# Kernel tuning notes

Measured on AMD Instinct MI355X. Metric: run time of the kernel, lower is better.

The kernel has to match this reference:

```python
import jax, jax.numpy as jnp
import numpy as np

B, T, E, H = 4, 2048, 1024, 16
HD = E // H  # 64


def setup_inputs() -> dict:
    key = jax.random.key(0)
    ks = jax.random.split(key, 7)
    s = 0.02
    return {
        "values": jax.random.normal(ks[0], (B, T, E), jnp.float32),
        "keys": jax.random.normal(ks[1], (B, T, E), jnp.float32),
        "query": jax.random.normal(ks[2], (B, T, E), jnp.float32),
        "Wv": jax.random.normal(ks[3], (HD, HD), jnp.float32) * s,
        "Wk": jax.random.normal(ks[4], (HD, HD), jnp.float32) * s,
        "Wq": jax.random.normal(ks[5], (HD, HD), jnp.float32) * s,
        "Wo": jax.random.normal(ks[6], (E, E), jnp.float32) * s,
    }


def _proj_split(x, W):
    # x: [B,T,E] -> per-head projection with shared [HD,HD] weight -> [B,H,T,HD]
    xh = x.reshape(B, T, H, HD)
    return jnp.einsum("bthd,ed->bhte", xh, W)  # torch Linear: x @ W.T


def reference(values, keys, query, Wv, Wk, Wq, Wo):
    v = _proj_split(values, Wv)   # [B,H,T,HD]
    k = _proj_split(keys, Wk)
    q = _proj_split(query, Wq)
    scale = 1.0 / np.sqrt(HD).astype(np.float32)
    scores = jnp.einsum("bhqd,bhkd->bhqk", q, k) * scale  # [B,H,T,T]
    probs = jax.nn.softmax(scores, axis=-1)
    attn = jnp.einsum("bhqk,bhkd->bhqd", probs, v)        # [B,H,T,HD]
    out = attn.transpose(0, 2, 1, 3).reshape(B, T, E)      # combine heads
    return out @ Wo.T
```

## Files before the change

kernel.cpp:

```cpp
#include <hip/hip_runtime.h>


typedef __bf16 bf16x8 __attribute__((ext_vector_type(8)));
typedef float f32x4 __attribute__((ext_vector_type(4)));
typedef float f32x16 __attribute__((ext_vector_type(16)));
typedef unsigned int u32x2v __attribute__((ext_vector_type(2)));
typedef unsigned int u32x4v __attribute__((ext_vector_type(4)));

#define DEVI static __device__ __forceinline__

constexpr int Bc = 4, Tc = 2048, Ec = 1024, HDc = 64;
constexpr int BHc = 64;

DEVI unsigned short f2bf(float f) {
  unsigned int u = __builtin_bit_cast(unsigned int, f);
  u += 0x7fffu + ((u >> 16) & 1u);
  return (unsigned short)(u >> 16);
}

DEVI int swzf(int row) { return (row & 7) ^ ((row >> 3) & 3); }

DEVI bf16x8 lds_frag(const unsigned short* base, int row, int chunk) {
  const char* p = reinterpret_cast<const char*>(base) + row * 128 + ((chunk ^ swzf(row)) * 16);
  return *reinterpret_cast<const bf16x8*>(p);
}
DEVI void lds_store16(unsigned short* base, int row, int ci, uint4 v) {
  char* p = reinterpret_cast<char*>(base) + row * 128 + ((ci ^ swzf(row)) * 16);
  *reinterpret_cast<uint4*>(p) = v;
}
DEVI uint4 pack8(float4 a, float4 b) {
  uint4 o;
  o.x = f2bf(a.x) | ((unsigned)f2bf(a.y) << 16);
  o.y = f2bf(a.z) | ((unsigned)f2bf(a.w) << 16);
  o.z = f2bf(b.x) | ((unsigned)f2bf(b.y) << 16);
  o.w = f2bf(b.z) | ((unsigned)f2bf(b.w) << 16);
  return o;
}

DEVI unsigned cvt_pk_bf16(float lo, float hi) {
  unsigned r;
  asm("v_cvt_pk_bf16_f32 %0, %1, %2" : "=v"(r) : "v"(lo), "v"(hi));
  return r;
}
DEVI float exp2_fast(float x) {
  float r;
  asm("v_exp_f32 %0, %1" : "=v"(r) : "v"(x));
  return r;
}
DEVI void plswap(unsigned& a, unsigned& b) {
#if __has_builtin(__builtin_amdgcn_permlane32_swap)
  u32x2v r = __builtin_amdgcn_permlane32_swap(a, b, false, false);
  a = r.x; b = r.y;
#else
  int lane = threadIdx.x & 63;
  unsigned sa = (unsigned)__shfl_xor((int)a, 32), sb = (unsigned)__shfl_xor((int)b, 32);
  unsigned na = (lane < 32) ? a : sb;
  unsigned nb = (lane < 32) ? sa : b;
  a = na; b = nb;
#endif
}
DEVI float halfsum(float x) {
  unsigned a = __builtin_bit_cast(unsigned, x), b = a;
  plswap(a, b);
  return __builtin_bit_cast(float, a) + __builtin_bit_cast(float, b);
}

DEVI void gload16(const unsigned short* g, unsigned short* l) {
  __builtin_amdgcn_global_load_lds(
      (const __attribute__((address_space(1))) void*)g,
      (__attribute__((address_space(3))) void*)l, 16, 0, 0);
}

__global__ __launch_bounds__(256) void proj3_kernel(
    const float* __restrict__ xv, const float* __restrict__ xk,
    const float* __restrict__ xq, const float* __restrict__ Wv,
    const float* __restrict__ Wk, const float* __restrict__ Wq,
    const float* __restrict__ Wo, unsigned short* __restrict__ ov,
    unsigned short* __restrict__ ok, unsigned short* __restrict__ oq,
    unsigned short* __restrict__ wob, float qscale) {
  if (blockIdx.z == 3) {
    int cb = blockIdx.y * (int)gridDim.x + blockIdx.x;
    if (cb < 1024) {
      size_t i = (size_t)cb * 1024 + (size_t)threadIdx.x * 4;
      float4 f = *reinterpret_cast<const float4*>(Wo + i);
      uint2 o;
      o.x = f2bf(f.x) | ((unsigned)f2bf(f.y) << 16);
      o.y = f2bf(f.z) | ((unsigned)f2bf(f.w) << 16);
      *reinterpret_cast<uint2*>(wob + i) = o;
    }
    return;
  }
  const int which = blockIdx.z;
  const float* x = which == 0 ? xv : which == 1 ? xk : xq;
  const float* W = which == 0 ? Wv : which == 1 ? Wk : Wq;
  unsigned short* out = which == 0 ? ov : which == 1 ? ok : oq;
  const int transposed = (which == 0);
  const float wscale = (which == 2) ? qscale : 1.0f;

  __shared__ __align__(16) unsigned short Xl[64 * 64];
  __shared__ __align__(16) unsigned short Wl[64 * 64];
  const int tid = threadIdx.x;
  const int bh = blockIdx.y, t0 = blockIdx.x * 64;
  const int b = bh >> 4, h = bh & 15;
  const float* xbase = x + (size_t)(b * Tc + t0) * Ec + h * HDc;

#pragma unroll
  for (int it = 0; it < 2; ++it) {
    int ch = tid + it * 256;
    int row = ch >> 3, ci = ch & 7;
    float4 wa = *reinterpret_cast<const float4*>(W + row * 64 + ci * 8);
    float4 wb = *reinterpret_cast<const float4*>(W + row * 64 + ci * 8 + 4);
    wa.x *= wscale; wa.y *= wscale; wa.z *= wscale; wa.w *= wscale;
    wb.x *= wscale; wb.y *= wscale; wb.z *= wscale; wb.w *= wscale;
    lds_store16(Wl, row, ci, pack8(wa, wb));
    float4 xa = *reinterpret_cast<const float4*>(xbase + (size_t)row * Ec + ci * 8);
    float4 xb = *reinterpret_cast<const float4*>(xbase + (size_t)row * Ec + ci * 8 + 4);
    lds_store16(Xl, row, ci, pack8(xa, xb));
  }
  __syncthreads();

  const int lane = tid & 63, wv = tid >> 6;
  const int c16 = lane & 15, hi = lane >> 4;
  f32x4 acc[4];
#pragma unroll
  for (int nb = 0; nb < 4; ++nb) acc[nb] = {0.f, 0.f, 0.f, 0.f};
  if (!transposed) {
#pragma unroll
    for (int c = 0; c < 2; ++c) {
      bf16x8 aX = lds_frag(Xl, 16 * wv + c16, 4 * c + hi);
#pragma unroll
      for (int nb = 0; nb < 4; ++nb) {
        bf16x8 bW = lds_frag(Wl, 16 * nb + c16, 4 * c + hi);
        acc[nb] = __builtin_amdgcn_mfma_f32_16x16x32_bf16(aX, bW, acc[nb], 0, 0, 0);
      }
    }
#pragma unroll
    for (int nb = 0; nb < 4; ++nb)
#pragma unroll
      for (int r = 0; r < 4; ++r) {
        int t = t0 + 16 * wv + 4 * hi + r;
        int e = 16 * nb + c16;
        out[(size_t)(bh * Tc + t) * HDc + e] = f2bf(acc[nb][r]);
      }
  } else {
#pragma unroll
    for (int c = 0; c < 2; ++c) {
      bf16x8 aW = lds_frag(Wl, 16 * wv + c16, 4 * c + hi);
#pragma unroll
      for (int nb = 0; nb < 4; ++nb) {
        bf16x8 bX = lds_frag(Xl, 16 * nb + c16, 4 * c + hi);
        acc[nb] = __builtin_amdgcn_mfma_f32_16x16x32_bf16(aW, bX, acc[nb], 0, 0, 0);
      }
    }
#pragma unroll
    for (int nb = 0; nb < 4; ++nb)
#pragma unroll
      for (int r = 0; r < 4; ++r) {
        int e = 16 * wv + 4 * hi + r;
        int t = t0 + 16 * nb + c16;
        out[(size_t)(bh * HDc + e) * Tc + t] = f2bf(acc[nb][r]);
      }
  }
}

DEVI void stage_kv(const unsigned short* __restrict__ Kp,
                   const unsigned short* __restrict__ Vp, int kt,
                   unsigned short* Kl, unsigned short* Vl, int wv, int lane) {
#pragma unroll
  for (int j = 0; j < 2; ++j) {
    const int base = (4 * j + wv) * 64;
    const int slot = base + lane;
    const int row = slot >> 3;
    const int sc = ((slot & 7) ^ swzf(row)) * 8;
    gload16(Kp + (size_t)(kt * 64 + row) * 64 + sc, Kl + base * 8);
    gload16(Vp + (size_t)row * Tc + kt * 64 + sc, Vl + base * 8);
  }
}

DEVI float exp_sum_pf(f32x16& s0, f32x16& s1, bf16x8 pf[4]) {
#pragma unroll
  for (int i = 0; i < 16; ++i) s0[i] = exp2_fast(s0[i]);
#pragma unroll
  for (int i = 0; i < 16; ++i) s1[i] = exp2_fast(s1[i]);
  float t[16];
#pragma unroll
  for (int i = 0; i < 16; ++i) t[i] = s0[i] + s1[i];
#pragma unroll
  for (int i = 0; i < 8; ++i) t[i] += t[i + 8];
#pragma unroll
  for (int i = 0; i < 4; ++i) t[i] += t[i + 4];
  float rs = (t[0] + t[1]) + (t[2] + t[3]);
  unsigned w0[8], w1[8];
#pragma unroll
  for (int i = 0; i < 8; ++i) w0[i] = cvt_pk_bf16(s0[2 * i], s0[2 * i + 1]);
#pragma unroll
  for (int i = 0; i < 8; ++i) w1[i] = cvt_pk_bf16(s1[2 * i], s1[2 * i + 1]);
  plswap(w0[0], w0[2]); plswap(w0[1], w0[3]); plswap(w0[4], w0[6]); plswap(w0[5], w0[7]);
  plswap(w1[0], w1[2]); plswap(w1[1], w1[3]); plswap(w1[4], w1[6]); plswap(w1[5], w1[7]);
  pf[0] = __builtin_bit_cast(bf16x8, (u32x4v){w0[0], w0[1], w0[2], w0[3]});
  pf[1] = __builtin_bit_cast(bf16x8, (u32x4v){w0[4], w0[5], w0[6], w0[7]});
  pf[2] = __builtin_bit_cast(bf16x8, (u32x4v){w1[0], w1[1], w1[2], w1[3]});
  pf[3] = __builtin_bit_cast(bf16x8, (u32x4v){w1[4], w1[5], w1[6], w1[7]});
  return rs;
}

__global__ __launch_bounds__(256, 2) void attn_kernel(
    const unsigned short* __restrict__ Qb_, const unsigned short* __restrict__ Kb_,
    const unsigned short* __restrict__ Vtb_, unsigned short* __restrict__ O) {
  __shared__ __align__(16) unsigned short KV[4][2][64 * 64];
  const int tid = threadIdx.x, lane = tid & 63, wv = tid >> 6;
  const int c32 = lane & 31, hi = lane >> 5;
  const int flat = blockIdx.y * (int)gridDim.x + blockIdx.x;
  const int logical = (flat & 7) * 64 + (flat >> 3);
  const int q0 = (logical & 7) * 256, bh = logical >> 3;
  const int b = bh >> 4, h = bh & 15;
  const unsigned short* Qp = Qb_ + (size_t)bh * Tc * HDc;
  const unsigned short* Kp = Kb_ + (size_t)bh * Tc * HDc;
  const unsigned short* Vp = Vtb_ + (size_t)bh * HDc * Tc;

  const int tA = q0 + 64 * wv + c32, tB = tA + 32;
  bf16x8 qfA[4], qfB[4];
#pragma unroll
  for (int c = 0; c < 4; ++c) {
    qfA[c] = *reinterpret_cast<const bf16x8*>(Qp + (size_t)tA * HDc + 16 * c + 8 * hi);
    qfB[c] = *reinterpret_cast<const bf16x8*>(Qp + (size_t)tB * HDc + 16 * c + 8 * hi);
  }

  stage_kv(Kp, Vp, 0, KV[0][0], KV[0][1], wv, lane);
  stage_kv(Kp, Vp, 1, KV[1][0], KV[1][1], wv, lane);

  f32x16 aA0, aA1, aB0, aB1, zv;
#pragma unroll
  for (int i = 0; i < 16; ++i) {
    aA0[i] = 0.f; aA1[i] = 0.f; aB0[i] = 0.f; aB1[i] = 0.f; zv[i] = 0.f;
  }
  float lA = 0.f, lB = 0.f;

  auto tile = [&](const unsigned short* Kl, const unsigned short* Vl) {
    f32x16 sA0, sA1, sB0, sB1;
    __builtin_amdgcn_s_setprio(1);
    {
      bf16x8 k0 = lds_frag(Kl, c32, hi);
      sA0 = __builtin_amdgcn_mfma_f32_32x32x16_bf16(k0, qfA[0], zv, 0, 0, 0);
      sB0 = __builtin_amdgcn_mfma_f32_32x32x16_bf16(k0, qfB[0], zv, 0, 0, 0);
      bf16x8 k1 = lds_frag(Kl, 32 + c32, hi);
      sA1 = __builtin_amdgcn_mfma_f32_32x32x16_bf16(k1, qfA[0], zv, 0, 0, 0);
      sB1 = __builtin_amdgcn_mfma_f32_32x32x16_bf16(k1, qfB[0], zv, 0, 0, 0);
    }
#pragma unroll
    for (int c = 1; c < 4; ++c) {
      bf16x8 k0 = lds_frag(Kl, c32, 2 * c + hi);
      sA0 = __builtin_amdgcn_mfma_f32_32x32x16_bf16(k0, qfA[c], sA0, 0, 0, 0);
      sB0 = __builtin_amdgcn_mfma_f32_32x32x16_bf16(k0, qfB[c], sB0, 0, 0, 0);
      bf16x8 k1 = lds_frag(Kl, 32 + c32, 2 * c + hi);
      sA1 = __builtin_amdgcn_mfma_f32_32x32x16_bf16(k1, qfA[c], sA1, 0, 0, 0);
      sB1 = __builtin_amdgcn_mfma_f32_32x32x16_bf16(k1, qfB[c], sB1, 0, 0, 0);
    }
    __builtin_amdgcn_s_setprio(0);
    bf16x8 pfA[4], pfB[4];
    lA += exp_sum_pf(sA0, sA1, pfA);
    lB += exp_sum_pf(sB0, sB1, pfB);
    __builtin_amdgcn_s_setprio(1);
#pragma unroll
    for (int ks = 0; ks < 4; ++ks) {
      bf16x8 v0 = lds_frag(Vl, c32, 2 * ks + hi);
      aA0 = __builtin_amdgcn_mfma_f32_32x32x16_bf16(v0, pfA[ks], aA0, 0, 0, 0);
      aB0 = __builtin_amdgcn_mfma_f32_32x32x16_bf16(v0, pfB[ks], aB0, 0, 0, 0);
      bf16x8 v1 = lds_frag(Vl, 32 + c32, 2 * ks + hi);
      aA1 = __builtin_amdgcn_mfma_f32_32x32x16_bf16(v1, pfA[ks], aA1, 0, 0, 0);
      aB1 = __builtin_amdgcn_mfma_f32_32x32x16_bf16(v1, pfB[ks], aB1, 0, 0, 0);
    }
    __builtin_amdgcn_s_setprio(0);
  };

  constexpr int NT = Tc / 64;
  for (int t = 0; t < NT; ++t) {
    if (t + 2 < NT) {
      stage_kv(Kp, Vp, t + 2, KV[(t + 2) & 3][0], KV[(t + 2) & 3][1], wv, lane);
      asm volatile("s_waitcnt vmcnt(8)" ::: "memory");
    } else if (t + 1 < NT) {
      asm volatile("s_waitcnt vmcnt(4)" ::: "memory");
    } else {
      asm volatile("s_waitcnt vmcnt(0)" ::: "memory");
    }
    __builtin_amdgcn_s_barrier();
    tile(KV[t & 3][0], KV[t & 3][1]);
  }

  {
    const float rl = 1.0f / halfsum(lA);
    unsigned short* orow = O + (size_t)(b * Tc + tA) * Ec + h * HDc;
#pragma unroll
    for (int rq = 0; rq < 4; ++rq) {
      uint2 p0, p1;
      p0.x = cvt_pk_bf16(aA0[4 * rq] * rl, aA0[4 * rq + 1] * rl);
      p0.y = cvt_pk_bf16(aA0[4 * rq + 2] * rl, aA0[4 * rq + 3] * rl);
      *reinterpret_cast<uint2*>(orow + 8 * rq + 4 * hi) = p0;
      p1.x = cvt_pk_bf16(aA1[4 * rq] * rl, aA1[4 * rq + 1] * rl);
      p1.y = cvt_pk_bf16(aA1[4 * rq + 2] * rl, aA1[4 * rq + 3] * rl);
      *reinterpret_cast<uint2*>(orow + 32 + 8 * rq + 4 * hi) = p1;
    }
  }
  {
    const float rl = 1.0f / halfsum(lB);
    unsigned short* orow = O + (size_t)(b * Tc + tB) * Ec + h * HDc;
#pragma unroll
    for (int rq = 0; rq < 4; ++rq) {
      uint2 p0, p1;
      p0.x = cvt_pk_bf16(aB0[4 * rq] * rl, aB0[4 * rq + 1] * rl);
      p0.y = cvt_pk_bf16(aB0[4 * rq + 2] * rl, aB0[4 * rq + 3] * rl);
      *reinterpret_cast<uint2*>(orow + 8 * rq + 4 * hi) = p0;
      p1.x = cvt_pk_bf16(aB1[4 * rq] * rl, aB1[4 * rq + 1] * rl);
      p1.y = cvt_pk_bf16(aB1[4 * rq + 2] * rl, aB1[4 * rq + 3] * rl);
      *reinterpret_cast<uint2*>(orow + 32 + 8 * rq + 4 * hi) = p1;
    }
  }
}

DEVI void stage_ab(const unsigned short* __restrict__ Ap,
                   const unsigned short* __restrict__ Bp, int kt,
                   unsigned short* Al, unsigned short* Bl, int wv, int lane) {
#pragma unroll
  for (int j = 0; j < 4; ++j) {
    const int base = (4 * j + wv) * 64;
    const int slot = base + lane;
    const int row = slot >> 3;
    const int sc = ((slot & 7) ^ swzf(row)) * 8;
    gload16(Ap + (size_t)row * Ec + kt * 64 + sc, Al + base * 8);
    gload16(Bp + (size_t)row * Ec + kt * 64 + sc, Bl + base * 8);
  }
}

__global__ __launch_bounds__(256, 2) void ogemm_kernel(
    const unsigned short* __restrict__ A, const unsigned short* __restrict__ Bw,
    float* __restrict__ out) {
  __shared__ __align__(16) unsigned short Al[2][128 * 64];
  __shared__ __align__(16) unsigned short Bl[2][128 * 64];
  const int tid = threadIdx.x, lane = tid & 63, wv = tid >> 6;
  const int c32 = lane & 31, hi = lane >> 5;
  const int flat = blockIdx.y * (int)gridDim.x + blockIdx.x;
  const int logical = (flat & 7) * 64 + (flat >> 3);
  const int n0 = (logical & 7) * 128, m0 = (logical >> 3) * 128;
  const int wr = wv >> 1, wc = wv & 1;
  const unsigned short* Ap = A + (size_t)m0 * Ec;
  const unsigned short* Bp = Bw + (size_t)n0 * Ec;

  f32x16 acc[2][2];
#pragma unroll
  for (int mi = 0; mi < 2; ++mi)
#pragma unroll
    for (int ni = 0; ni < 2; ++ni)
#pragma unroll
      for (int i = 0; i < 16; ++i) acc[mi][ni][i] = 0.f;

  auto gtile = [&](const unsigned short* Alc, const unsigned short* Blc) {
    __builtin_amdgcn_s_setprio(1);
#pragma unroll
    for (int kc = 0; kc < 4; ++kc) {
      bf16x8 x0 = lds_frag(Alc, 64 * wr + c32, 2 * kc + hi);
      bf16x8 x1 = lds_frag(Alc, 64 * wr + 32 + c32, 2 * kc + hi);
      bf16x8 y0 = lds_frag(Blc, 64 * wc + c32, 2 * kc + hi);
      bf16x8 y1 = lds_frag(Blc, 64 * wc + 32 + c32, 2 * kc + hi);
      acc[0][0] = __builtin_amdgcn_mfma_f32_32x32x16_bf16(x0, y0, acc[0][0], 0, 0, 0);
      acc[0][1] = __builtin_amdgcn_mfma_f32_32x32x16_bf16(x0, y1, acc[0][1], 0, 0, 0);
      acc[1][0] = __builtin_amdgcn_mfma_f32_32x32x16_bf16(x1, y0, acc[1][0], 0, 0, 0);
      acc[1][1] = __builtin_amdgcn_mfma_f32_32x32x16_bf16(x1, y1, acc[1][1], 0, 0, 0);
    }
    __builtin_amdgcn_s_setprio(0);
  };

  stage_ab(Ap, Bp, 0, Al[0], Bl[0], wv, lane);
  __syncthreads();
  for (int kt = 0; kt < Ec / 64; kt += 2) {
    stage_ab(Ap, Bp, kt + 1, Al[1], Bl[1], wv, lane);
    gtile(Al[0], Bl[0]);
    __syncthreads();
    if (kt + 2 < Ec / 64) stage_ab(Ap, Bp, kt + 2, Al[0], Bl[0], wv, lane);
    gtile(Al[1], Bl[1]);
    __syncthreads();
  }

  const int nb = n0 + 64 * wc + c32;
  const int mb = m0 + 64 * wr + 4 * hi;
#pragma unroll
  for (int mi = 0; mi < 2; ++mi)
#pragma unroll
    for (int ni = 0; ni < 2; ++ni)
#pragma unroll
      for (int rq = 0; rq < 4; ++rq)
#pragma unroll
        for (int j = 0; j < 4; ++j) {
          int mrow = mb + 32 * mi + 8 * rq + j;
          out[(size_t)mrow * Ec + nb + 32 * ni] = acc[mi][ni][4 * rq + j];
        }
}

extern "C" void kernel_launch(void* const* d_in, const int* in_sizes, int n_in,
                              void* d_out, int out_size, void* d_ws, size_t ws_size,
                              hipStream_t stream) {
  (void)in_sizes; (void)n_in; (void)out_size; (void)ws_size;
  const float* values = (const float*)d_in[0];
  const float* keys   = (const float*)d_in[1];
  const float* query  = (const float*)d_in[2];
  const float* Wv = (const float*)d_in[3];
  const float* Wk = (const float*)d_in[4];
  const float* Wq = (const float*)d_in[5];
  const float* Wo = (const float*)d_in[6];
  float* out = (float*)d_out;

  char* ws = (char*)d_ws;
  constexpr size_t SZ = (size_t)BHc * Tc * HDc * 2;
  unsigned short* qb  = (unsigned short*)(ws + 0 * SZ);
  unsigned short* kb  = (unsigned short*)(ws + 1 * SZ);
  unsigned short* vt  = (unsigned short*)(ws + 2 * SZ);
  unsigned short* at  = (unsigned short*)(ws + 3 * SZ);
  unsigned short* wob = (unsigned short*)(ws + 4 * SZ);

  dim3 blk(256);
  proj3_kernel<<<dim3(Tc / 64, BHc, 4), blk, 0, stream>>>(
      values, keys, query, Wv, Wk, Wq, Wo, vt, kb, qb, wob,
      0.18033688011112042f);
  attn_kernel<<<dim3(Tc / 256, BHc), blk, 0, stream>>>(qb, kb, vt, at);
  ogemm_kernel<<<dim3(Ec / 128, (Bc * Tc) / 128), blk, 0, stream>>>(at, wob, out);
}
```

Baseline: 124.2 us.

## Shrink output GEMM tile to 128x64 for more blocks and occupancy

```diff
diff --git a/kernel.cpp b/kernel.cpp
--- a/kernel.cpp
+++ b/kernel.cpp
@@ -327,44 +327,38 @@
     const int row = slot >> 3;
     const int sc = ((slot & 7) ^ swzf(row)) * 8;
     gload16(Ap + (size_t)row * Ec + kt * 64 + sc, Al + base * 8);
-    gload16(Bp + (size_t)row * Ec + kt * 64 + sc, Bl + base * 8);
-  }
-}
-
-__global__ __launch_bounds__(256, 2) void ogemm_kernel(
+    if (j < 2) gload16(Bp + (size_t)row * Ec + kt * 64 + sc, Bl + base * 8);
+  }
+}
+
+__global__ __launch_bounds__(256, 3) void ogemm_kernel(
     const unsigned short* __restrict__ A, const unsigned short* __restrict__ Bw,
     float* __restrict__ out) {
   __shared__ __align__(16) unsigned short Al[2][128 * 64];
-  __shared__ __align__(16) unsigned short Bl[2][128 * 64];
+  __shared__ __align__(16) unsigned short Bl[2][64 * 64];
   const int tid = threadIdx.x, lane = tid & 63, wv = tid >> 6;
   const int c32 = lane & 31, hi = lane >> 5;
   const int flat = blockIdx.y * (int)gridDim.x + blockIdx.x;
-  const int logical = (flat & 7) * 64 + (flat >> 3);
-  const int n0 = (logical & 7) * 128, m0 = (logical >> 3) * 128;
-  const int wr = wv >> 1, wc = wv & 1;
+  const int logical = (flat & 7) * 128 + (flat >> 3);
+  const int n0 = (logical & 15) * 64, m0 = (logical >> 4) * 128;
   const unsigned short* Ap = A + (size_t)m0 * Ec;
   const unsigned short* Bp = Bw + (size_t)n0 * Ec;
 
-  f32x16 acc[2][2];
-#pragma unroll
-  for (int mi = 0; mi < 2; ++mi)
-#pragma unroll
-    for (int ni = 0; ni < 2; ++ni)
-#pragma unroll
-      for (int i = 0; i < 16; ++i) acc[mi][ni][i] = 0.f;
+  f32x16 acc[2];
+#pragma unroll
+  for (int ni = 0; ni < 2; ++ni)
+#pragma unroll
+    for (int i = 0; i < 16; ++i) acc[ni][i] = 0.f;
 
   auto gtile = [&](const unsigned short* Alc, const unsigned short* Blc) {
     __builtin_amdgcn_s_setprio(1);
 #pragma unroll
     for (int kc = 0; kc < 4; ++kc) {
-      bf16x8 x0 = lds_frag(Alc, 64 * wr + c32, 2 * kc + hi);
-      bf16x8 x1 = lds_frag(Alc, 64 * wr + 32 + c32, 2 * kc + hi);
-      bf16x8 y0 = lds_frag(Blc, 64 * wc + c32, 2 * kc + hi);
-      bf16x8 y1 = lds_frag(Blc, 64 * wc + 32 + c32, 2 * kc + hi);
-      acc[0][0] = __builtin_amdgcn_mfma_f32_32x32x16_bf16(x0, y0, acc[0][0], 0, 0, 0);
-      acc[0][1] = __builtin_amdgcn_mfma_f32_32x32x16_bf16(x0, y1, acc[0][1], 0, 0, 0);
-      acc[1][0] = __builtin_amdgcn_mfma_f32_32x32x16_bf16(x1, y0, acc[1][0], 0, 0, 0);
-      acc[1][1] = __builtin_amdgcn_mfma_f32_32x32x16_bf16(x1, y1, acc[1][1], 0, 0, 0);
+      bf16x8 x  = lds_frag(Alc, 32 * wv + c32, 2 * kc + hi);
+      bf16x8 y0 = lds_frag(Blc, c32, 2 * kc + hi);
+      bf16x8 y1 = lds_frag(Blc, 32 + c32, 2 * kc + hi);
+      acc[0] = __builtin_amdgcn_mfma_f32_32x32x16_bf16(x, y0, acc[0], 0, 0, 0);
+      acc[1] = __builtin_amdgcn_mfma_f32_32x32x16_bf16(x, y1, acc[1], 0, 0, 0);
     }
     __builtin_amdgcn_s_setprio(0);
   };
@@ -380,19 +374,16 @@
     __syncthreads();
   }
 
-  const int nb = n0 + 64 * wc + c32;
-  const int mb = m0 + 64 * wr + 4 * hi;
-#pragma unroll
-  for (int mi = 0; mi < 2; ++mi)
-#pragma unroll
-    for (int ni = 0; ni < 2; ++ni)
-#pragma unroll
-      for (int rq = 0; rq < 4; ++rq)
-#pragma unroll
-        for (int j = 0; j < 4; ++j) {
-          int mrow = mb + 32 * mi + 8 * rq + j;
-          out[(size_t)mrow * Ec + nb + 32 * ni] = acc[mi][ni][4 * rq + j];
-        }
+  const int mb = m0 + 32 * wv + 4 * hi;
+#pragma unroll
+  for (int ni = 0; ni < 2; ++ni)
+#pragma unroll
+    for (int rq = 0; rq < 4; ++rq)
+#pragma unroll
+      for (int j = 0; j < 4; ++j) {
+        int mrow = mb + 8 * rq + j;
+        out[(size_t)mrow * Ec + n0 + 32 * ni + c32] = acc[ni][4 * rq + j];
+      }
 }
 
 extern "C" void kernel_launch(void* const* d_in, const int* in_sizes, int n_in,
@@ -421,5 +412,5 @@
       values, keys, query, Wv, Wk, Wq, Wo, vt, kb, qb, wob,
       0.18033688011112042f);
   attn_kernel<<<dim3(Tc / 256, BHc), blk, 0, stream>>>(qb, kb, vt, at);
-  ogemm_kernel<<<dim3(Ec / 128, (Bc * Tc) / 128), blk, 0, stream>>>(at, wob, out);
-}
+  ogemm_kernel<<<dim3(16, (Bc * Tc) / 128), blk, 0, stream>>>(at, wob, out);
+}
```

After: 131.6 us. +5.9%, slower.
